# Performance work log

Hardware: AMD Instinct MI355X
Metric: run time of the kernel (lower is better)

Reference implementation:

```python
import jax, jax.numpy as jnp
import numpy as np

DIM = 1024
HEADS = 16
HEAD_DIM = DIM // HEADS
B, N = 2, 2048


def setup_inputs() -> dict:
    key = jax.random.key(0)
    k1, k2, k3, k4 = jax.random.split(key, 4)
    x = jax.random.normal(k1, (B, N, DIM), dtype=jnp.float32)
    # torch Linear weights: shape (out_features, in_features), y = x @ W.T + b
    w_qkv = jax.random.normal(k2, (3 * DIM, DIM), dtype=jnp.float32) * (DIM ** -0.5)
    w_proj = jax.random.normal(k3, (DIM, DIM), dtype=jnp.float32) * (DIM ** -0.5)
    b_proj = jax.random.normal(k4, (DIM,), dtype=jnp.float32) * 0.01
    return {"x": x, "w_qkv": w_qkv, "w_proj": w_proj, "b_proj": b_proj}


def reference(x, w_qkv, w_proj, b_proj):
    Bb, Nn, D = x.shape
    scale = HEAD_DIM ** -0.5
    qkv = x @ w_qkv.T                                # [B, N, 3D]
    qkv = qkv.reshape(Bb, Nn, 3, HEADS, HEAD_DIM)
    qkv = jnp.transpose(qkv, (2, 0, 3, 1, 4))        # [3, B, H, N, hd]
    q, k, v = qkv[0], qkv[1], qkv[2]
    attn = jnp.einsum('bhqd,bhkd->bhqk', q, k) * scale
    attn = jax.nn.softmax(attn, axis=-1)
    out = jnp.einsum('bhqk,bhkd->bhqd', attn, v)     # [B, H, N, hd]
    out = jnp.transpose(out, (0, 2, 1, 3)).reshape(Bb, Nn, D)
    return out @ w_proj.T + b_proj
```

## Files before the change

### kernel.cpp

```cpp
#include <hip/hip_runtime.h>
#include <hip/hip_bf16.h>
#include <cstdint>
#include <cstddef>

using u16 = unsigned short;
using u32 = uint32_t;
using f32x4  = __attribute__((ext_vector_type(4))) float;
using bf16x8 = __attribute__((ext_vector_type(8))) __bf16;
using s16x4  = __attribute__((ext_vector_type(4))) short;

#define D_MODEL 1024
#define N_HEADS 16
#define HD      64
#define SEQ     2048
#define QKV_LD  3072
#define K2SCALE 0.18033688011112042f

__device__ __forceinline__ u16 f2b(float f) {
  union { float f; u32 u; } v; v.f = f;
  u32 r = 0x7FFFu + ((v.u >> 16) & 1u);
  return (u16)((v.u + r) >> 16);
}

__device__ __forceinline__ u32 pkbf16(float a, float b) {
  union { __hip_bfloat162 h; u32 u; } c;
  c.h = __float22bfloat162_rn(float2{a, b});
  return c.u;
}

#define MFMA16(A, B, C) __builtin_amdgcn_mfma_f32_16x16x16bf16_1k(A, B, C, 0, 0, 0)

__device__ __forceinline__ void gld16(const u16* g, u16* l) {
  __builtin_amdgcn_global_load_lds(
      (const __attribute__((address_space(1))) void*)g,
      (__attribute__((address_space(3))) void*)l, 16, 0, 0);
}

__global__ void cast3_bf16(const float* __restrict__ x, const float* __restrict__ wq,
                           const float* __restrict__ wp, u16* __restrict__ dst) {
  int i = blockIdx.x * blockDim.x + threadIdx.x;
  const float* src;
  int off;
  if (blockIdx.x < 4096)      { src = x;  off = 0; }
  else if (blockIdx.x < 7168) { src = wq; off = 4096 * 256; }
  else                        { src = wp; off = 7168 * 256; }
  float4 f = ((const float4*)src)[i - off];
  u32 lo = pkbf16(f.x, f.y), hi = pkbf16(f.z, f.w);
  uint2 o = {lo, hi};
  ((uint2*)dst)[i] = o;
}

template<int OUTMODE, int MT>
__launch_bounds__(256, 3)
__global__ void gemm_nt(const u16* __restrict__ A, const u16* __restrict__ B,
                        u16* __restrict__ Ob, float* __restrict__ Of,
                        const float* __restrict__ bias, int N, int K) {
  __shared__ __attribute__((aligned(16))) u16 sA[2][MT * 32];
  __shared__ __attribute__((aligned(16))) u16 sB[2][128 * 32];

  const int tid  = threadIdx.x;
  const int lane = tid & 63;
  const int w    = tid >> 6;
  const int qd   = lane >> 4;
  const int ln   = lane & 15;
  constexpr int MI = MT / 32;
  const int wm   = (w >> 1) * (MT / 2);
  const int wn   = (w & 1) * 64;
  const int m0   = blockIdx.y * MT;
  const int n0   = blockIdx.x * 128;

  auto stage = [&](int kk, int buf) {
    int k0 = kk * 32;
    #pragma unroll
    for (int c = 0; c < MT / 64; ++c) {
      int sbase = w * MT + c * 64;
      int s = sbase + lane;
      int row = s >> 2, col = (s & 3) * 8;
      gld16(A + (size_t)(m0 + row) * K + k0 + col, &sA[buf][sbase * 8]);
    }
    #pragma unroll
    for (int c = 0; c < 2; ++c) {
      int sbase = w * 128 + c * 64;
      int s = sbase + lane;
      int row = s >> 2, col = (s & 3) * 8;
      gld16(B + (size_t)(n0 + row) * K + k0 + col, &sB[buf][sbase * 8]);
    }
  };

  f32x4 acc[MI][4] = {};
  const int NK = K >> 5;
  stage(0, 0);

  for (int kk = 0; kk < NK; ++kk) {
    const int cur = kk & 1;
    __syncthreads();
    if (kk + 1 < NK) stage(kk + 1, cur ^ 1);

    bf16x8 af[MI], bfm[4];
    #pragma unroll
    for (int i = 0; i < MI; ++i)
      af[i] = *(const bf16x8*)&sA[cur][(wm + i * 16 + ln) * 32 + qd * 8];
    #pragma unroll
    for (int j = 0; j < 4; ++j)
      bfm[j] = *(const bf16x8*)&sB[cur][(wn + j * 16 + ln) * 32 + qd * 8];
    #pragma unroll
    for (int i = 0; i < MI; ++i)
      #pragma unroll
      for (int j = 0; j < 4; ++j)
        acc[i][j] = __builtin_amdgcn_mfma_f32_16x16x32_bf16(af[i], bfm[j], acc[i][j], 0, 0, 0);
  }

  #pragma unroll
  for (int i = 0; i < MI; ++i) {
    #pragma unroll
    for (int j = 0; j < 4; ++j) {
      #pragma unroll
      for (int r = 0; r < 4; ++r) {
        int row = m0 + wm + i * 16 + qd * 4 + r;
        int col = n0 + wn + j * 16 + ln;
        float v = acc[i][j][r];
        if (OUTMODE == 0) {
          if (col < D_MODEL) v *= K2SCALE;
          Ob[(size_t)row * N + col] = f2b(v);
        } else {
          Of[(size_t)row * N + col] = v + bias[col];
        }
      }
    }
  }
}

__launch_bounds__(256, 2)
__global__ void attn_kernel(const u16* __restrict__ qkv, u16* __restrict__ outb) {
  __shared__ __attribute__((aligned(16))) u16 sK[2][2][128 * 32];
  __shared__ __attribute__((aligned(16))) u32 sVT[2][64 * 64];

  const int tid  = threadIdx.x;
  const int lane = tid & 63;
  const int w    = tid >> 6;
  const int qd   = lane >> 4;
  const int ln   = lane & 15;
  const int qp   = blockIdx.x;
  const int h    = blockIdx.y & 15;
  const int b    = blockIdx.y >> 4;
  const size_t tokbase = (size_t)b * SEQ;
  const int q0   = qp * 128;
  const int qoff = h * HD;
  const int koff = D_MODEL + h * HD;
  const int voff = 2 * D_MODEL + h * HD;

  bf16x8 aq[2][2];
  #pragma unroll
  for (int c2 = 0; c2 < 2; ++c2)
    #pragma unroll
    for (int hf = 0; hf < 2; ++hf)
      aq[c2][hf] = *(const bf16x8*)(qkv + (tokbase + q0 + c2 * 64 + w * 16 + ln) * QKV_LD
                                    + qoff + hf * 32 + qd * 8);

  auto stageK = [&](int kt, int buf) {
    #pragma unroll
    for (int hf = 0; hf < 2; ++hf)
      #pragma unroll
      for (int c = 0; c < 2; ++c) {
        int sbase = w * 128 + c * 64;
        int s = sbase + lane;
        int row = s >> 2, col = (s & 3) * 8;
        gld16(qkv + (tokbase + kt * 128 + row) * QKV_LD + koff + hf * 32 + col,
              &sK[buf][hf][sbase * 8]);
      }
  };
  auto loadV = [&](int kt, uint4* va, uint4* vb) {
    #pragma unroll
    for (int it = 0; it < 2; ++it) {
      int j = it * 256 + tid;
      int tp = j & 63, d0 = (j >> 6) * 8;
      const u16* g0 = qkv + (tokbase + kt * 128 + tp * 2) * QKV_LD + voff + d0;
      va[it] = *(const uint4*)g0;
      vb[it] = *(const uint4*)(g0 + QKV_LD);
    }
  };
  auto writeV = [&](int buf, const uint4* va, const uint4* vb) {
    #pragma unroll
    for (int it = 0; it < 2; ++it) {
      int j = it * 256 + tid;
      int tp = j & 63, d0 = (j >> 6) * 8;
      const u32* a  = (const u32*)&va[it];
      const u32* bb = (const u32*)&vb[it];
      #pragma unroll
      for (int e = 0; e < 4; ++e) {
        sVT[buf][(d0 + 2 * e    ) * 64 + (tp ^ (e << 4)    )] =
            __builtin_amdgcn_perm(bb[e], a[e], 0x05040100u);
        sVT[buf][(d0 + 2 * e + 1) * 64 + (tp ^ (e << 4) ^ 8)] =
            __builtin_amdgcn_perm(bb[e], a[e], 0x07060302u);
      }
    }
  };

  stageK(0, 0);
  uint4 va[2], vb[2];
  loadV(0, va, vb);
  writeV(0, va, vb);
  loadV(1, va, vb);

  f32x4 accOT[2][4] = {};
  float psum[2] = {0.f, 0.f};
  const int tsw = (ln & 7) << 3;

  for (int kt = 0; kt < 16; ++kt) {
    const int cur = kt & 1, nxt = cur ^ 1;
    __syncthreads();
    if (kt < 15) { stageK(kt + 1, nxt); writeV(nxt, va, vb); }
    if (kt < 14) { loadV(kt + 2, va, vb); }

    #pragma unroll
    for (int cb = 0; cb < 8; ++cb) {
      bf16x8 ak0 = *(const bf16x8*)&sK[cur][0][(cb * 16 + ln) * 32 + qd * 8];
      bf16x8 ak1 = *(const bf16x8*)&sK[cur][1][(cb * 16 + ln) * 32 + qd * 8];
      f32x4 st[2];
      #pragma unroll
      for (int c2 = 0; c2 < 2; ++c2) {
        f32x4 z = {0.f, 0.f, 0.f, 0.f};
        f32x4 t = __builtin_amdgcn_mfma_f32_16x16x32_bf16(ak0, aq[c2][0], z, 0, 0, 0);
        st[c2]  = __builtin_amdgcn_mfma_f32_16x16x32_bf16(ak1, aq[c2][1], t, 0, 0, 0);
      }
      s16x4 pf[2];
      #pragma unroll
      for (int c2 = 0; c2 < 2; ++c2) {
        float p0 = __builtin_amdgcn_exp2f(st[c2][0]);
        float p1 = __builtin_amdgcn_exp2f(st[c2][1]);
        float p2 = __builtin_amdgcn_exp2f(st[c2][2]);
        float p3 = __builtin_amdgcn_exp2f(st[c2][3]);
        psum[c2] += (p0 + p1) + (p2 + p3);
        union { u32 d[2]; s16x4 v; } pk;
        pk.d[0] = pkbf16(p0, p1);
        pk.d[1] = pkbf16(p2, p3);
        pf[c2] = pk.v;
      }
      #pragma unroll
      for (int ob = 0; ob < 4; ++ob) {
        s16x4 vf = *(const s16x4*)&sVT[cur][(ob * 16 + ln) * 64
                                           + ((cb * 8 + qd * 2) ^ tsw)];
        accOT[0][ob] = MFMA16(vf, pf[0], accOT[0][ob]);
        accOT[1][ob] = MFMA16(vf, pf[1], accOT[1][ob]);
      }
    }
  }

  #pragma unroll
  for (int c2 = 0; c2 < 2; ++c2) {
    float s = psum[c2];
    s += __shfl_xor(s, 16, 64);
    s += __shfl_xor(s, 32, 64);
    psum[c2] = 1.0f / s;
  }

  u16* sOut = (u16*)&sK[0][0][0];
  __syncthreads();
  #pragma unroll
  for (int c2 = 0; c2 < 2; ++c2)
    #pragma unroll
    for (int ob = 0; ob < 4; ++ob) {
      u32 lo = pkbf16(accOT[c2][ob][0] * psum[c2], accOT[c2][ob][1] * psum[c2]);
      u32 hi = pkbf16(accOT[c2][ob][2] * psum[c2], accOT[c2][ob][3] * psum[c2]);
      ((u32*)sOut)[(c2 * 64 + w * 16 + ln) * 36 + ob * 8 + qd * 2    ] = lo;
      ((u32*)sOut)[(c2 * 64 + w * 16 + ln) * 36 + ob * 8 + qd * 2 + 1] = hi;
    }
  __syncthreads();
  #pragma unroll
  for (int it = 0; it < 4; ++it) {
    int idx = it * 256 + tid;
    int token = idx >> 3, chunk = idx & 7;
    uint4 v = *(const uint4*)&sOut[token * 72 + chunk * 8];
    *(uint4*)&outb[(tokbase + q0 + token) * D_MODEL + h * HD + chunk * 8] = v;
  }
}

extern "C" void kernel_launch(void* const* d_in, const int* in_sizes, int n_in,
                              void* d_out, int out_size, void* d_ws, size_t ws_size,
                              hipStream_t stream) {
  const float* x      = (const float*)d_in[0];
  const float* w_qkv  = (const float*)d_in[1];
  const float* w_proj = (const float*)d_in[2];
  const float* b_proj = (const float*)d_in[3];
  float* out = (float*)d_out;

  u16* ws     = (u16*)d_ws;
  u16* xb     = ws;
  u16* wqkvb  = xb    + (size_t)4096 * 1024;
  u16* wprojb = wqkvb + (size_t)3072 * 1024;
  u16* qkvb   = wprojb + (size_t)1024 * 1024;
  u16* attnb  = qkvb  + (size_t)4096 * 3072;

  cast3_bf16<<<8192, 256, 0, stream>>>(x, w_qkv, w_proj, xb);

  gemm_nt<0, 128><<<dim3(24, 32), 256, 0, stream>>>(xb, wqkvb, qkvb, nullptr, nullptr, 3072, 1024);

  attn_kernel<<<dim3(16, 32), 256, 0, stream>>>(qkvb, attnb);

  gemm_nt<1, 64><<<dim3(8, 64), 256, 0, stream>>>(attnb, wprojb, nullptr, out, b_proj, 1024, 1024);
}
```

Measured before the change: 194.6 us.

## Fuse fp32-to-bf16 cast into GEMM tile loads and drop cast kernel

Removes the separate cast kernel and its bf16 workspace copies of x, w_qkv and w_proj. The GEMM staging now loads fp32 tiles, converts them to bf16 in registers and stores them to LDS. This cuts one launch and a full read/write pass, but it doubles the global bytes per tile load, repeats the conversion for every block that reuses a tile, and replaces async global-to-LDS loads with synchronous register loads, which can hurt latency hiding.

```diff
diff --git a/kernel.cpp b/kernel.cpp
--- a/kernel.cpp
+++ b/kernel.cpp
@@ -36,27 +36,18 @@
       (__attribute__((address_space(3))) void*)l, 16, 0, 0);
 }
 
-__global__ void cast3_bf16(const float* __restrict__ x, const float* __restrict__ wq,
-                           const float* __restrict__ wp, u16* __restrict__ dst) {
-  int i = blockIdx.x * blockDim.x + threadIdx.x;
-  const float* src;
-  int off;
-  if (blockIdx.x < 4096)      { src = x;  off = 0; }
-  else if (blockIdx.x < 7168) { src = wq; off = 4096 * 256; }
-  else                        { src = wp; off = 7168 * 256; }
-  float4 f = ((const float4*)src)[i - off];
-  u32 lo = pkbf16(f.x, f.y), hi = pkbf16(f.z, f.w);
-  uint2 o = {lo, hi};
-  ((uint2*)dst)[i] = o;
-}
-
-template<int OUTMODE, int MT>
+template<int OUTMODE, int MT, int CASTA, int CASTB>
 __launch_bounds__(256, 3)
-__global__ void gemm_nt(const u16* __restrict__ A, const u16* __restrict__ B,
+__global__ void gemm_nt(const void* __restrict__ Av, const void* __restrict__ Bv,
                         u16* __restrict__ Ob, float* __restrict__ Of,
                         const float* __restrict__ bias, int N, int K) {
   __shared__ __attribute__((aligned(16))) u16 sA[2][MT * 32];
   __shared__ __attribute__((aligned(16))) u16 sB[2][128 * 32];
+
+  const u16*   Ab = (const u16*)Av;
+  const float* Af = (const float*)Av;
+  const u16*   Bb = (const u16*)Bv;
+  const float* Bf = (const float*)Bv;
 
   const int tid  = threadIdx.x;
   const int lane = tid & 63;
@@ -73,17 +64,33 @@
     int k0 = kk * 32;
     #pragma unroll
     for (int c = 0; c < MT / 64; ++c) {
-      int sbase = w * MT + c * 64;
-      int s = sbase + lane;
+      int s = w * MT + c * 64 + lane;
       int row = s >> 2, col = (s & 3) * 8;
-      gld16(A + (size_t)(m0 + row) * K + k0 + col, &sA[buf][sbase * 8]);
+      if (CASTA) {
+        const float* g = Af + (size_t)(m0 + row) * K + k0 + col;
+        float4 f0 = *(const float4*)g;
+        float4 f1 = *(const float4*)(g + 4);
+        uint4 o = {pkbf16(f0.x, f0.y), pkbf16(f0.z, f0.w),
+                   pkbf16(f1.x, f1.y), pkbf16(f1.z, f1.w)};
+        *(uint4*)&sA[buf][s * 8] = o;
+      } else {
+        gld16(Ab + (size_t)(m0 + row) * K + k0 + col, &sA[buf][(w * MT + c * 64) * 8]);
+      }
     }
     #pragma unroll
     for (int c = 0; c < 2; ++c) {
-      int sbase = w * 128 + c * 64;
-      int s = sbase + lane;
+      int s = w * 128 + c * 64 + lane;
       int row = s >> 2, col = (s & 3) * 8;
-      gld16(B + (size_t)(n0 + row) * K + k0 + col, &sB[buf][sbase * 8]);
+      if (CASTB) {
+        const float* g = Bf + (size_t)(n0 + row) * K + k0 + col;
+        float4 f0 = *(const float4*)g;
+        float4 f1 = *(const float4*)(g + 4);
+        uint4 o = {pkbf16(f0.x, f0.y), pkbf16(f0.z, f0.w),
+                   pkbf16(f1.x, f1.y), pkbf16(f1.z, f1.w)};
+        *(uint4*)&sB[buf][s * 8] = o;
+      } else {
+        gld16(Bb + (size_t)(n0 + row) * K + k0 + col, &sB[buf][(w * 128 + c * 64) * 8]);
+      }
     }
   };
 
@@ -285,17 +292,14 @@
   float* out = (float*)d_out;
 
   u16* ws     = (u16*)d_ws;
-  u16* xb     = ws;
-  u16* wqkvb  = xb    + (size_t)4096 * 1024;
-  u16* wprojb = wqkvb + (size_t)3072 * 1024;
-  u16* qkvb   = wprojb + (size_t)1024 * 1024;
-  u16* attnb  = qkvb  + (size_t)4096 * 3072;
-
-  cast3_bf16<<<8192, 256, 0, stream>>>(x, w_qkv, w_proj, xb);
-
-  gemm_nt<0, 128><<<dim3(24, 32), 256, 0, stream>>>(xb, wqkvb, qkvb, nullptr, nullptr, 3072, 1024);
+  u16* qkvb   = ws;
+  u16* attnb  = qkvb + (size_t)4096 * 3072;
+
+  gemm_nt<0, 128, 1, 1><<<dim3(24, 32), 256, 0, stream>>>(
+      x, w_qkv, qkvb, nullptr, nullptr, 3072, 1024);
 
   attn_kernel<<<dim3(16, 32), 256, 0, stream>>>(qkvb, attnb);
 
-  gemm_nt<1, 64><<<dim3(8, 64), 256, 0, stream>>>(attnb, wprojb, nullptr, out, b_proj, 1024, 1024);
-}
+  gemm_nt<1, 64, 0, 1><<<dim3(8, 64), 256, 0, stream>>>(
+      attnb, w_proj, nullptr, out, b_proj, 1024, 1024);
+}
```

Result: slower. 222.4 us (+14.3%).
